# Performance work log

Measured on AMD Instinct MI355X. Metric: run time of the kernel, lower is better.

## Reference

```python
import jax, jax.numpy as jnp
import numpy as np

N_O = 50000
N_Q = 50000
E = 1_600_000
POS_DIM = 3
LATENT = 128
HEADS = 4
HEAD_DIM = 32
EDGE_IN = 3 * POS_DIM  # ['rel','q_pos','o_pos']


def setup_inputs() -> dict:
    key = jax.random.key(0)
    ks = jax.random.split(key, 12)
    h_obs = jax.random.normal(ks[0], (N_O, LATENT), dtype=jnp.float32)
    pos_obs = jax.random.uniform(ks[1], (N_O, POS_DIM), dtype=jnp.float32)
    pos_query = jax.random.uniform(ks[2], (N_Q, POS_DIM), dtype=jnp.float32)
    src = jax.random.randint(ks[3], (E,), 0, N_O, dtype=jnp.int32)
    dst = jnp.sort(jax.random.randint(ks[4], (E,), 0, N_Q, dtype=jnp.int32))
    s = 0.05
    W1 = jax.random.normal(ks[5], (EDGE_IN, LATENT), dtype=jnp.float32) * s
    b1 = jnp.zeros((LATENT,), dtype=jnp.float32)
    W2 = jax.random.normal(ks[6], (LATENT, HEADS), dtype=jnp.float32) * s
    b2 = jnp.zeros((HEADS,), dtype=jnp.float32)
    Wv = jax.random.normal(ks[7], (LATENT, HEADS * HEAD_DIM), dtype=jnp.float32) * s
    bv = jnp.zeros((HEADS * HEAD_DIM,), dtype=jnp.float32)
    log_sigma = jnp.float32(-2.0)
    return {"h_obs": h_obs, "pos_obs": pos_obs, "pos_query": pos_query,
            "src": src, "dst": dst,
            "W1": W1, "b1": b1, "W2": W2, "b2": b2,
            "Wv": Wv, "bv": bv, "log_sigma": log_sigma}


def _forward(h_obs, pos_obs, pos_query, src, dst, W1, b1, W2, b2, Wv, bv, log_sigma):
    pos_o = pos_obs[src]                      # [E, P]
    pos_q = pos_query[dst]                    # [E, P]
    rel = pos_q - pos_o
    edge_attr = jnp.concatenate([rel, pos_q, pos_o], axis=-1)   # [E, 3P]
    hid = jax.nn.relu(edge_attr @ W1 + b1)                      # [E, LATENT]
    logits = hid @ W2 + b2                                      # [E, H]
    dist2 = jnp.sum(rel * rel, axis=-1, keepdims=True)          # [E, 1]
    sigma = jnp.exp(log_sigma) + 1e-6
    logits = logits - dist2 / (2.0 * sigma * sigma)             # kernel log-weight
    # segment softmax over edges grouped by dst
    n_q = pos_query.shape[0]
    m = jax.ops.segment_max(logits, dst, num_segments=n_q)      # [N_q, H]
    ex = jnp.exp(logits - m[dst])
    denom = jax.ops.segment_sum(ex, dst, num_segments=n_q)      # [N_q, H]
    attn = ex / (denom[dst] + 1e-16)                            # [E, H]
    v = (h_obs @ Wv + bv).reshape(-1, HEADS, HEAD_DIM)          # [N_o, H, D]
    msg = attn[:, :, None] * v[src]                             # [E, H, D]
    out = jax.ops.segment_sum(msg, dst, num_segments=n_q)       # [N_q, H, D]
    return out.reshape(n_q, HEADS * HEAD_DIM)


def reference(h_obs, pos_obs, pos_query, src, dst, W1, b1, W2, b2, Wv, bv, log_sigma):
    return _forward(h_obs, pos_obs, pos_query, src, dst, W1, b1, W2, b2, Wv, bv, log_sigma)
```

## Files before the change

kernel.cpp:

```cpp
#include <hip/hip_runtime.h>
#include <hip/hip_bf16.h>
#include <cstdint>
#include <cstddef>

#define N_O 50000
#define N_Q 50000
#define NE  1600000

#define EDGE_BLOCKS  (NE / 64)
#define VP_BLOCKS    ((N_O + 31) / 32)
#define RP_BLOCKS    ((N_Q + 128) / 128)
#define WCAP 264

#define WVP_OFF   38608768u
#define WVP_BYTES 65536u

typedef __attribute__((ext_vector_type(8)))  short short8;
typedef __attribute__((ext_vector_type(16))) float f32x16;

__device__ inline unsigned short f2bf(float x) {
    __hip_bfloat16 hb = __float2bfloat16(x);
    return *reinterpret_cast<unsigned short*>(&hb);
}

__device__ inline unsigned pk2(float a, float b) {
    __hip_bfloat162 t = __float22bfloat162_rn(make_float2(a, b));
    return *reinterpret_cast<unsigned*>(&t);
}

__global__ void pack_kernel(const float* __restrict__ W1, const float* __restrict__ b1,
                            const float* __restrict__ W2, const float* __restrict__ b2,
                            const float* __restrict__ log_sigma,
                            const float* __restrict__ Wv,
                            unsigned short* __restrict__ W1cT,
                            unsigned short* __restrict__ W2tb,
                            float* __restrict__ scal,
                            unsigned short* __restrict__ WvPhi,
                            unsigned short* __restrict__ WvPlo,
                            int vp_mfma) {
    int j = threadIdx.x;
    if (blockIdx.x == 0) {
        if (j < 128) {
            #pragma unroll
            for (int a = 0; a < 3; ++a) {
                W1cT[j * 8 + a]     = f2bf(W1[(3 + a) * 128 + j] + W1[a * 128 + j]);
                W1cT[j * 8 + 3 + a] = f2bf(W1[(6 + a) * 128 + j] - W1[a * 128 + j]);
            }
            W1cT[j * 8 + 6] = f2bf(b1[j]);
            W1cT[j * 8 + 7] = 0;
            #pragma unroll
            for (int hd = 0; hd < 4; ++hd)
                W2tb[hd * 128 + j] = f2bf(W2[j * 4 + hd]);
        } else if (j == 128) {
            float sigma = expf(log_sigma[0]) + 1e-6f;
            scal[0] = 1.0f / (2.0f * sigma * sigma);
            scal[1] = b2[0]; scal[2] = b2[1]; scal[3] = b2[2]; scal[4] = b2[3];
        }
    } else if (vp_mfma) {
        int fr = (blockIdx.x - 1) * 256 + j;
        int lane = fr & 63, i = lane & 31, g = lane >> 5;
        int ks = (fr >> 6) & 7, c = fr >> 9;
        #pragma unroll
        for (int e = 0; e < 8; ++e) {
            float w = Wv[(size_t)(16 * ks + 8 * g + e) * 128 + 32 * c + i];
            unsigned short hi = f2bf(w);
            float rem = w - __uint_as_float(((unsigned)hi) << 16);
            WvPhi[fr * 8 + e] = hi;
            WvPlo[fr * 8 + e] = f2bf(rem);
        }
    }
}

__device__ void rowptr_body(int bid, const int* __restrict__ dst, int* __restrict__ rp) {
    int q = bid * 128 + threadIdx.x;
    if (q > N_Q) return;
    int lo = 0, hi = NE;
    while (lo < hi) {
        int mid = (lo + hi) >> 1;
        if (dst[mid] < q) lo = mid + 1; else hi = mid;
    }
    rp[q] = lo;
}

__device__ void vproj_mfma_body(int tile, const float* __restrict__ h,
                                const unsigned short* __restrict__ WvPhi,
                                const unsigned short* __restrict__ WvPlo,
                                const float* __restrict__ bv,
                                unsigned short* __restrict__ v) {
    int lane = threadIdx.x & 63, wave = threadIdx.x >> 6;
    int i = lane & 31, g = lane >> 5;
    int n = tile * 32 + i;
    bool nok = (n < N_O);
    const float* hrow = h + (size_t)n * 128;

    short8 Bhi[8], Blo[8];
    #pragma unroll
    for (int ks = 0; ks < 8; ++ks) {
        float4 u0 = make_float4(0.f, 0.f, 0.f, 0.f), u1 = u0;
        if (nok) {
            u0 = *(const float4*)(hrow + 16 * ks + 8 * g);
            u1 = *(const float4*)(hrow + 16 * ks + 8 * g + 4);
        }
        float x[8] = {u0.x, u0.y, u0.z, u0.w, u1.x, u1.y, u1.z, u1.w};
        union { unsigned u[4]; short8 s; } ph, pl;
        #pragma unroll
        for (int p = 0; p < 4; ++p) {
            ph.u[p] = pk2(x[2 * p], x[2 * p + 1]);
            float e0 = x[2 * p]     - __uint_as_float(ph.u[p] << 16);
            float e1 = x[2 * p + 1] - __uint_as_float(ph.u[p] & 0xffff0000u);
            pl.u[p] = pk2(e0, e1);
        }
        Bhi[ks] = ph.s; Blo[ks] = pl.s;
    }

    #pragma unroll 1
    for (int cc = 0; cc < 2; ++cc) {
        int c = 2 * wave + cc;
        f32x16 acc;
        #pragma unroll
        for (int k = 0; k < 16; ++k) acc[k] = 0.f;
        #pragma unroll
        for (int ks = 0; ks < 8; ++ks) {
            int fr = (c * 8 + ks) * 64 + lane;
            short8 Ahi = *(const short8*)(WvPhi + fr * 8);
            short8 Alo = *(const short8*)(WvPlo + fr * 8);
            acc = __builtin_amdgcn_mfma_f32_32x32x16_bf16(Ahi, Bhi[ks], acc, 0, 0, 0);
            acc = __builtin_amdgcn_mfma_f32_32x32x16_bf16(Ahi, Blo[ks], acc, 0, 0, 0);
            acc = __builtin_amdgcn_mfma_f32_32x32x16_bf16(Alo, Bhi[ks], acc, 0, 0, 0);
        }
        if (nok) {
            #pragma unroll
            for (int q = 0; q < 4; ++q) {
                int vc = 32 * c + 8 * q + 4 * g;
                float4 bq = *(const float4*)(bv + vc);
                uint2 ov;
                ov.x = pk2(acc[4 * q + 0] + bq.x, acc[4 * q + 1] + bq.y);
                ov.y = pk2(acc[4 * q + 2] + bq.z, acc[4 * q + 3] + bq.w);
                *(uint2*)(v + (size_t)n * 128 + vc) = ov;
            }
        }
    }
}

__device__ void vproj_f32_body(int bid, const float* __restrict__ h,
                               const float* __restrict__ Wv,
                               const float* __restrict__ bv,
                               unsigned short* __restrict__ v,
                               float* Ash ) {
    int t = threadIdx.x;
    int n0 = bid * 32;
    #pragma unroll
    for (int rep = 0; rep < 8; ++rep) {
        int idx = rep * 128 + t;
        int row = idx >> 5, c4 = (idx & 31) * 4;
        float4 val = make_float4(0.f, 0.f, 0.f, 0.f);
        if (n0 + row < N_O) val = *(const float4*)(h + (size_t)(n0 + row) * 128 + c4);
        float* d = &Ash[row * 132 + c4];
        d[0] = val.x; d[1] = val.y; d[2] = val.z; d[3] = val.w;
    }
    __syncthreads();

    int cg = t & 15, rg = t >> 4;
    int c0 = cg * 8, r0 = rg * 4;
    float acc[4][8];
    #pragma unroll
    for (int i = 0; i < 4; ++i)
        #pragma unroll
        for (int j = 0; j < 8; ++j) acc[i][j] = 0.f;

    const float4* Wv4 = (const float4*)Wv;
    for (int k = 0; k < 128; ++k) {
        float4 b0 = Wv4[k * 32 + cg * 2];
        float4 b1v = Wv4[k * 32 + cg * 2 + 1];
        float bb[8] = {b0.x, b0.y, b0.z, b0.w, b1v.x, b1v.y, b1v.z, b1v.w};
        #pragma unroll
        for (int i = 0; i < 4; ++i) {
            float a = Ash[(r0 + i) * 132 + k];
            #pragma unroll
            for (int j = 0; j < 8; ++j) acc[i][j] += a * bb[j];
        }
    }

    float bvv[8];
    #pragma unroll
    for (int j = 0; j < 8; ++j) bvv[j] = bv[c0 + j];
    #pragma unroll
    for (int i = 0; i < 4; ++i) {
        int n = n0 + r0 + i;
        if (n < N_O) {
            uint4 o;
            o.x = pk2(acc[i][0] + bvv[0], acc[i][1] + bvv[1]);
            o.y = pk2(acc[i][2] + bvv[2], acc[i][3] + bvv[3]);
            o.z = pk2(acc[i][4] + bvv[4], acc[i][5] + bvv[5]);
            o.w = pk2(acc[i][6] + bvv[6], acc[i][7] + bvv[7]);
            *(uint4*)(v + (size_t)n * 128 + c0) = o;
        }
    }
}

__device__ void edge_body(int bid, const float* __restrict__ pos_obs,
                          const float* __restrict__ pos_query,
                          const int* __restrict__ src, const int* __restrict__ dst,
                          const unsigned short* __restrict__ W1cT,
                          const unsigned short* __restrict__ W2tb,
                          const float* __restrict__ scal,
                          float* __restrict__ logitsT,
                          unsigned char* smem ) {
    int t = threadIdx.x;
    int wave = t >> 6, lane = t & 63;
    int i = lane & 31, h = lane >> 5;
    unsigned char* myrow = smem + wave * 8448 + i * 264;

    short8 zero8;
    #pragma unroll
    for (int k = 0; k < 8; ++k) zero8[k] = 0;

    short8 a1[4];
    #pragma unroll
    for (int b = 0; b < 4; ++b)
        a1[b] = (h == 0) ? *(const short8*)(W1cT + (32 * b + i) * 8) : zero8;

    short8 a2[8];
    #pragma unroll
    for (int m = 0; m < 8; ++m)
        a2[m] = (i < 4) ? *(const short8*)(W2tb + i * 128 + m * 16 + h * 8) : zero8;

    int e = bid * 64 + wave * 32 + i;
    int s = src[e], d = dst[e];
    float pox = pos_obs[s * 3 + 0], poy = pos_obs[s * 3 + 1], poz = pos_obs[s * 3 + 2];
    float pqx = pos_query[d * 3 + 0], pqy = pos_query[d * 3 + 1], pqz = pos_query[d * 3 + 2];
    float rx = pqx - pox, ry = pqy - poy, rz = pqz - poz;
    float dist2 = rx * rx + ry * ry + rz * rz;

    short8 bea = zero8;
    if (h == 0) {
        bea[0] = (short)f2bf(pqx); bea[1] = (short)f2bf(pqy); bea[2] = (short)f2bf(pqz);
        bea[3] = (short)f2bf(pox); bea[4] = (short)f2bf(poy); bea[5] = (short)f2bf(poz);
        bea[6] = (short)0x3F80;
        bea[7] = 0;
    }

    f32x16 c1[4];
    #pragma unroll
    for (int b = 0; b < 4; ++b) {
        #pragma unroll
        for (int k = 0; k < 16; ++k) c1[b][k] = 0.0f;
        c1[b] = __builtin_amdgcn_mfma_f32_32x32x16_bf16(a1[b], bea, c1[b], 0, 0, 0);
    }

    #pragma unroll
    for (int b = 0; b < 4; ++b) {
        #pragma unroll
        for (int s_ = 0; s_ < 4; ++s_) {
            float x0 = fmaxf(c1[b][4 * s_ + 0], 0.f);
            float x1 = fmaxf(c1[b][4 * s_ + 1], 0.f);
            float x2 = fmaxf(c1[b][4 * s_ + 2], 0.f);
            float x3 = fmaxf(c1[b][4 * s_ + 3], 0.f);
            uint2 w;
            w.x = pk2(x0, x1);
            w.y = pk2(x2, x3);
            *(uint2*)(myrow + 64 * b + 16 * s_ + 8 * h) = w;
        }
    }

    f32x16 c2;
    #pragma unroll
    for (int k = 0; k < 16; ++k) c2[k] = 0.0f;
    #pragma unroll
    for (int m = 0; m < 8; ++m) {
        uint2 lo = *(const uint2*)(myrow + 32 * m + 16 * h);
        uint2 hi = *(const uint2*)(myrow + 32 * m + 16 * h + 8);
        union { unsigned int u[4]; short8 s; } bf;
        bf.u[0] = lo.x; bf.u[1] = lo.y; bf.u[2] = hi.x; bf.u[3] = hi.y;
        c2 = __builtin_amdgcn_mfma_f32_32x32x16_bf16(a2[m], bf.s, c2, 0, 0, 0);
    }

    if (h == 0) {
        float pen = dist2 * scal[0];
        logitsT[0 * NE + e] = c2[0] + scal[1] - pen;
        logitsT[1 * NE + e] = c2[1] + scal[2] - pen;
        logitsT[2 * NE + e] = c2[2] + scal[3] - pen;
        logitsT[3 * NE + e] = c2[3] + scal[4] - pen;
    }
}

__global__ __launch_bounds__(128) void fused_kernel(
        const float* __restrict__ pos_obs, const float* __restrict__ pos_query,
        const int* __restrict__ src, const int* __restrict__ dst,
        const unsigned short* __restrict__ W1cT,
        const unsigned short* __restrict__ W2tb,
        const float* __restrict__ scal, float* __restrict__ logitsT,
        const float* __restrict__ h_obs, const float* __restrict__ Wv,
        const float* __restrict__ bv, unsigned short* __restrict__ vbuf,
        int* __restrict__ rp,
        const unsigned short* __restrict__ WvPhi,
        const unsigned short* __restrict__ WvPlo,
        int vp_mfma) {
    __shared__ __align__(16) unsigned char smem[16896];
    int b = blockIdx.x;
    if (b < EDGE_BLOCKS) {
        edge_body(b, pos_obs, pos_query, src, dst, W1cT, W2tb, scal, logitsT, smem);
    } else if (b < EDGE_BLOCKS + VP_BLOCKS) {
        int tile = b - EDGE_BLOCKS;
        if (vp_mfma) vproj_mfma_body(tile, h_obs, WvPhi, WvPlo, bv, vbuf);
        else         vproj_f32_body(tile, h_obs, Wv, bv, vbuf, (float*)smem);
    } else {
        rowptr_body(b - EDGE_BLOCKS - VP_BLOCKS, dst, rp);
    }
}

__global__ __launch_bounds__(256) void attn_kernel(const __hip_bfloat162* __restrict__ vb,
                                                   const float* __restrict__ logitsT,
                                                   const int* __restrict__ src,
                                                   const int* __restrict__ rp,
                                                   float* __restrict__ out) {
    __shared__ __align__(16) float wsh[4 * 4 * WCAP];
    int t = threadIdx.x;
    int lane = t & 63, wave = t >> 6;
    int q = blockIdx.x * 4 + wave;
    int s0 = rp[q], s1 = rp[q + 1];
    int cnt = s1 - s0;
    int h = lane >> 4, i = lane & 15;
    const float* lp = logitsT + (size_t)h * NE;

    float m = -INFINITY;
    for (int e = s0 + i; e < s1; e += 16) m = fmaxf(m, lp[e]);
    #pragma unroll
    for (int off = 8; off; off >>= 1) m = fmaxf(m, __shfl_xor(m, off));

    float acc0 = 0.f, acc1 = 0.f, r;

    if (cnt <= 256) {
        int s0a = s0 & ~3;
        float* wpb = wsh + wave * (4 * WCAP) + h * WCAP;
        float sum = 0.f;
        for (int e = s0 + i; e < s1; e += 16) {
            float w = __expf(lp[e] - m);
            wpb[e - s0a] = w;
            sum += w;
        }
        #pragma unroll
        for (int off = 8; off; off >>= 1) sum += __shfl_xor(sum, off);
        r = 1.0f / (sum + 1e-16f);

        int e = s0;
        int e1 = (s0 + 3) & ~3; if (e1 > s1) e1 = s1;
        for (; e < e1; ++e) {
            float w = wpb[e - s0a];
            float2 f = __bfloat1622float2(vb[(size_t)src[e] * 64 + lane]);
            acc0 += w * f.x; acc1 += w * f.y;
        }
        for (; e + 4 <= s1; e += 4) {
            float4 w4 = *(const float4*)(wpb + (e - s0a));
            int4 s4 = *(const int4*)(src + e);
            float2 f0 = __bfloat1622float2(vb[(size_t)s4.x * 64 + lane]);
            float2 f1 = __bfloat1622float2(vb[(size_t)s4.y * 64 + lane]);
            float2 f2 = __bfloat1622float2(vb[(size_t)s4.z * 64 + lane]);
            float2 f3 = __bfloat1622float2(vb[(size_t)s4.w * 64 + lane]);
            acc0 += w4.x * f0.x + w4.y * f1.x + w4.z * f2.x + w4.w * f3.x;
            acc1 += w4.x * f0.y + w4.y * f1.y + w4.z * f2.y + w4.w * f3.y;
        }
        for (; e < s1; ++e) {
            float w = wpb[e - s0a];
            float2 f = __bfloat1622float2(vb[(size_t)src[e] * 64 + lane]);
            acc0 += w * f.x; acc1 += w * f.y;
        }
    } else {
        float sum = 0.f;
        for (int e = s0 + i; e < s1; e += 16) sum += __expf(lp[e] - m);
        #pragma unroll
        for (int off = 8; off; off >>= 1) sum += __shfl_xor(sum, off);
        r = 1.0f / (sum + 1e-16f);

        int e = s0;
        for (; e < s1 && (e & 3); ++e) {
            float w = __expf(lp[e] - m);
            float2 f = __bfloat1622float2(vb[(size_t)src[e] * 64 + lane]);
            acc0 += w * f.x; acc1 += w * f.y;
        }
        for (; e + 4 <= s1; e += 4) {
            float4 l4 = *(const float4*)(lp + e);
            int4 s4 = *(const int4*)(src + e);
            float w0 = __expf(l4.x - m);
            float w1 = __expf(l4.y - m);
            float w2 = __expf(l4.z - m);
            float w3 = __expf(l4.w - m);
            float2 f0 = __bfloat1622float2(vb[(size_t)s4.x * 64 + lane]);
            float2 f1 = __bfloat1622float2(vb[(size_t)s4.y * 64 + lane]);
            float2 f2 = __bfloat1622float2(vb[(size_t)s4.z * 64 + lane]);
            float2 f3 = __bfloat1622float2(vb[(size_t)s4.w * 64 + lane]);
            acc0 += w0 * f0.x + w1 * f1.x + w2 * f2.x + w3 * f3.x;
            acc1 += w0 * f0.y + w1 * f1.y + w2 * f2.y + w3 * f3.y;
        }
        for (; e < s1; ++e) {
            float w = __expf(lp[e] - m);
            float2 f = __bfloat1622float2(vb[(size_t)src[e] * 64 + lane]);
            acc0 += w * f.x; acc1 += w * f.y;
        }
    }
    *(float2*)(out + (size_t)q * 128 + lane * 2) = make_float2(acc0 * r, acc1 * r);
}

extern "C" void kernel_launch(void* const* d_in, const int* in_sizes, int n_in,
                              void* d_out, int out_size, void* d_ws, size_t ws_size,
                              hipStream_t stream) {
    const float* h_obs     = (const float*)d_in[0];
    const float* pos_obs   = (const float*)d_in[1];
    const float* pos_query = (const float*)d_in[2];
    const int*   src       = (const int*)d_in[3];
    const int*   dst       = (const int*)d_in[4];
    const float* W1        = (const float*)d_in[5];
    const float* b1        = (const float*)d_in[6];
    const float* W2        = (const float*)d_in[7];
    const float* b2        = (const float*)d_in[8];
    const float* Wv        = (const float*)d_in[9];
    const float* bv        = (const float*)d_in[10];
    const float* log_sigma = (const float*)d_in[11];
    float* out = (float*)d_out;

    char* ws = (char*)d_ws;
    int*            rp      = (int*)(ws + 0);
    float*          scal    = (float*)(ws + 200192);
    unsigned short* W1cT    = (unsigned short*)(ws + 200256);
    unsigned short* W2tb    = (unsigned short*)(ws + 202304);
    unsigned short* vbuf    = (unsigned short*)(ws + 208640);
    float*          logitsT = (float*)(ws + 13008768);
    unsigned short* WvPhi   = (unsigned short*)(ws + WVP_OFF);
    unsigned short* WvPlo   = (unsigned short*)(ws + WVP_OFF + 32768);

    int vp_mfma = (ws_size >= (size_t)WVP_OFF + WVP_BYTES) ? 1 : 0;

    hipLaunchKernelGGL(pack_kernel, dim3(9), dim3(256), 0, stream,
                       W1, b1, W2, b2, log_sigma, Wv, W1cT, W2tb, scal,
                       WvPhi, WvPlo, vp_mfma);
    hipLaunchKernelGGL(fused_kernel, dim3(EDGE_BLOCKS + VP_BLOCKS + RP_BLOCKS),
                       dim3(128), 0, stream,
                       pos_obs, pos_query, src, dst, W1cT, W2tb, scal, logitsT,
                       h_obs, Wv, bv, vbuf, rp, WvPhi, WvPlo, vp_mfma);
    hipLaunchKernelGGL(attn_kernel, dim3(N_Q / 4), dim3(256), 0, stream,
                       (const __hip_bfloat162*)vbuf, logitsT, src, rp, out);
}
```

Before: 244.7 us.

## Process 64 edges per wave in edge MLP and unroll gather loops by eight

The edge MLP now has each wave handle 64 edges instead of 32. Every lane gathers positions for its own edge, and lane shuffles feed two MFMA passes, so the per-edge index and position loads use the whole wave and the edge block count halves. The second-layer MFMA chain is split into two independent accumulators to shorten the dependency chain. The aggregation loops gain an eight-wide unrolled stage that keeps more independent gathers in flight. Launch bounds now request higher occupancy, which can increase register pressure.

```diff
diff --git a/kernel.cpp b/kernel.cpp
--- a/kernel.cpp
+++ b/kernel.cpp
@@ -7,7 +7,7 @@
 #define N_Q 50000
 #define NE  1600000
 
-#define EDGE_BLOCKS  (NE / 64)
+#define EDGE_BLOCKS  (NE / 128)
 #define VP_BLOCKS    ((N_O + 31) / 32)
 #define RP_BLOCKS    ((N_Q + 128) / 128)
 #define WCAP 264
@@ -215,76 +215,99 @@
     #pragma unroll
     for (int k = 0; k < 8; ++k) zero8[k] = 0;
 
-    short8 a1[4];
-    #pragma unroll
-    for (int b = 0; b < 4; ++b)
-        a1[b] = (h == 0) ? *(const short8*)(W1cT + (32 * b + i) * 8) : zero8;
-
-    short8 a2[8];
-    #pragma unroll
-    for (int m = 0; m < 8; ++m)
-        a2[m] = (i < 4) ? *(const short8*)(W2tb + i * 128 + m * 16 + h * 8) : zero8;
-
-    int e = bid * 64 + wave * 32 + i;
+    int e = bid * 128 + wave * 64 + lane;
     int s = src[e], d = dst[e];
     float pox = pos_obs[s * 3 + 0], poy = pos_obs[s * 3 + 1], poz = pos_obs[s * 3 + 2];
     float pqx = pos_query[d * 3 + 0], pqy = pos_query[d * 3 + 1], pqz = pos_query[d * 3 + 2];
     float rx = pqx - pox, ry = pqy - poy, rz = pqz - poz;
     float dist2 = rx * rx + ry * ry + rz * rz;
 
-    short8 bea = zero8;
-    if (h == 0) {
-        bea[0] = (short)f2bf(pqx); bea[1] = (short)f2bf(pqy); bea[2] = (short)f2bf(pqz);
-        bea[3] = (short)f2bf(pox); bea[4] = (short)f2bf(poy); bea[5] = (short)f2bf(poz);
-        bea[6] = (short)0x3F80;
-        bea[7] = 0;
-    }
-
-    f32x16 c1[4];
-    #pragma unroll
-    for (int b = 0; b < 4; ++b) {
-        #pragma unroll
-        for (int k = 0; k < 16; ++k) c1[b][k] = 0.0f;
-        c1[b] = __builtin_amdgcn_mfma_f32_32x32x16_bf16(a1[b], bea, c1[b], 0, 0, 0);
-    }
-
-    #pragma unroll
-    for (int b = 0; b < 4; ++b) {
-        #pragma unroll
-        for (int s_ = 0; s_ < 4; ++s_) {
-            float x0 = fmaxf(c1[b][4 * s_ + 0], 0.f);
-            float x1 = fmaxf(c1[b][4 * s_ + 1], 0.f);
-            float x2 = fmaxf(c1[b][4 * s_ + 2], 0.f);
-            float x3 = fmaxf(c1[b][4 * s_ + 3], 0.f);
-            uint2 w;
-            w.x = pk2(x0, x1);
-            w.y = pk2(x2, x3);
-            *(uint2*)(myrow + 64 * b + 16 * s_ + 8 * h) = w;
-        }
-    }
-
-    f32x16 c2;
-    #pragma unroll
-    for (int k = 0; k < 16; ++k) c2[k] = 0.0f;
-    #pragma unroll
-    for (int m = 0; m < 8; ++m) {
-        uint2 lo = *(const uint2*)(myrow + 32 * m + 16 * h);
-        uint2 hi = *(const uint2*)(myrow + 32 * m + 16 * h + 8);
-        union { unsigned int u[4]; short8 s; } bf;
-        bf.u[0] = lo.x; bf.u[1] = lo.y; bf.u[2] = hi.x; bf.u[3] = hi.y;
-        c2 = __builtin_amdgcn_mfma_f32_32x32x16_bf16(a2[m], bf.s, c2, 0, 0, 0);
-    }
-
-    if (h == 0) {
-        float pen = dist2 * scal[0];
-        logitsT[0 * NE + e] = c2[0] + scal[1] - pen;
-        logitsT[1 * NE + e] = c2[1] + scal[2] - pen;
-        logitsT[2 * NE + e] = c2[2] + scal[3] - pen;
-        logitsT[3 * NE + e] = c2[3] + scal[4] - pen;
-    }
-}
-
-__global__ __launch_bounds__(128) void fused_kernel(
+    unsigned pk[4];
+    pk[0] = pk2(pqx, pqy);
+    pk[1] = pk2(pqz, pox);
+    pk[2] = pk2(poy, poz);
+    pk[3] = 0x00003F80u;
+
+    unsigned pb[4];
+    #pragma unroll
+    for (int p = 0; p < 4; ++p) pb[p] = (unsigned)__shfl_xor((int)pk[p], 32);
+
+    union { unsigned u[4]; short8 s8; } beaA, beaB;
+    #pragma unroll
+    for (int p = 0; p < 4; ++p) {
+        beaA.u[p] = h ? 0u : pk[p];
+        beaB.u[p] = h ? 0u : pb[p];
+    }
+
+    short8 a1[4];
+    #pragma unroll
+    for (int b = 0; b < 4; ++b)
+        a1[b] = (h == 0) ? *(const short8*)(W1cT + (32 * b + i) * 8) : zero8;
+
+    short8 a2[8];
+    #pragma unroll
+    for (int m = 0; m < 8; ++m)
+        a2[m] = (i < 4) ? *(const short8*)(W2tb + i * 128 + m * 16 + h * 8) : zero8;
+
+    float headA[4], headB[4];
+
+    #pragma unroll
+    for (int set = 0; set < 2; ++set) {
+        const short8 bea = set ? beaB.s8 : beaA.s8;
+
+        f32x16 c1[4];
+        #pragma unroll
+        for (int b = 0; b < 4; ++b) {
+            #pragma unroll
+            for (int k = 0; k < 16; ++k) c1[b][k] = 0.0f;
+            c1[b] = __builtin_amdgcn_mfma_f32_32x32x16_bf16(a1[b], bea, c1[b], 0, 0, 0);
+        }
+
+        #pragma unroll
+        for (int b = 0; b < 4; ++b) {
+            #pragma unroll
+            for (int s_ = 0; s_ < 4; ++s_) {
+                float x0 = fmaxf(c1[b][4 * s_ + 0], 0.f);
+                float x1 = fmaxf(c1[b][4 * s_ + 1], 0.f);
+                float x2 = fmaxf(c1[b][4 * s_ + 2], 0.f);
+                float x3 = fmaxf(c1[b][4 * s_ + 3], 0.f);
+                uint2 w;
+                w.x = pk2(x0, x1);
+                w.y = pk2(x2, x3);
+                *(uint2*)(myrow + 64 * b + 16 * s_ + 8 * h) = w;
+            }
+        }
+
+        f32x16 cx, cy;
+        #pragma unroll
+        for (int k = 0; k < 16; ++k) { cx[k] = 0.0f; cy[k] = 0.0f; }
+        #pragma unroll
+        for (int m = 0; m < 8; m += 2) {
+            uint2 lo0 = *(const uint2*)(myrow + 32 * m + 16 * h);
+            uint2 hi0 = *(const uint2*)(myrow + 32 * m + 16 * h + 8);
+            uint2 lo1 = *(const uint2*)(myrow + 32 * (m + 1) + 16 * h);
+            uint2 hi1 = *(const uint2*)(myrow + 32 * (m + 1) + 16 * h + 8);
+            union { unsigned int u[4]; short8 s; } b0, b1u;
+            b0.u[0] = lo0.x; b0.u[1] = lo0.y; b0.u[2] = hi0.x; b0.u[3] = hi0.y;
+            b1u.u[0] = lo1.x; b1u.u[1] = lo1.y; b1u.u[2] = hi1.x; b1u.u[3] = hi1.y;
+            cx = __builtin_amdgcn_mfma_f32_32x32x16_bf16(a2[m],     b0.s,  cx, 0, 0, 0);
+            cy = __builtin_amdgcn_mfma_f32_32x32x16_bf16(a2[m + 1], b1u.s, cy, 0, 0, 0);
+        }
+        float* hd = set ? headB : headA;
+        #pragma unroll
+        for (int r = 0; r < 4; ++r) hd[r] = cx[r] + cy[r];
+    }
+
+    float pen = dist2 * scal[0];
+    #pragma unroll
+    for (int r = 0; r < 4; ++r) {
+        float vB = __shfl_xor(headB[r], 32);
+        float val = (h ? vB : headA[r]) + scal[1 + r] - pen;
+        logitsT[(size_t)r * NE + e] = val;
+    }
+}
+
+__global__ __launch_bounds__(128, 4) void fused_kernel(
         const float* __restrict__ pos_obs, const float* __restrict__ pos_query,
         const int* __restrict__ src, const int* __restrict__ dst,
         const unsigned short* __restrict__ W1cT,
@@ -350,6 +373,24 @@
             float2 f = __bfloat1622float2(vb[(size_t)src[e] * 64 + lane]);
             acc0 += w * f.x; acc1 += w * f.y;
         }
+        for (; e + 8 <= s1; e += 8) {
+            float4 wa = *(const float4*)(wpb + (e - s0a));
+            float4 wb = *(const float4*)(wpb + (e - s0a) + 4);
+            int4 sa = *(const int4*)(src + e);
+            int4 sb = *(const int4*)(src + e + 4);
+            float2 f0 = __bfloat1622float2(vb[(size_t)sa.x * 64 + lane]);
+            float2 f1 = __bfloat1622float2(vb[(size_t)sa.y * 64 + lane]);
+            float2 f2 = __bfloat1622float2(vb[(size_t)sa.z * 64 + lane]);
+            float2 f3 = __bfloat1622float2(vb[(size_t)sa.w * 64 + lane]);
+            float2 f4 = __bfloat1622float2(vb[(size_t)sb.x * 64 + lane]);
+            float2 f5 = __bfloat1622float2(vb[(size_t)sb.y * 64 + lane]);
+            float2 f6 = __bfloat1622float2(vb[(size_t)sb.z * 64 + lane]);
+            float2 f7 = __bfloat1622float2(vb[(size_t)sb.w * 64 + lane]);
+            acc0 += wa.x * f0.x + wa.y * f1.x + wa.z * f2.x + wa.w * f3.x
+                  + wb.x * f4.x + wb.y * f5.x + wb.z * f6.x + wb.w * f7.x;
+            acc1 += wa.x * f0.y + wa.y * f1.y + wa.z * f2.y + wa.w * f3.y
+                  + wb.x * f4.y + wb.y * f5.y + wb.z * f6.y + wb.w * f7.y;
+        }
         for (; e + 4 <= s1; e += 4) {
             float4 w4 = *(const float4*)(wpb + (e - s0a));
             int4 s4 = *(const int4*)(src + e);
@@ -377,6 +418,28 @@
             float w = __expf(lp[e] - m);
             float2 f = __bfloat1622float2(vb[(size_t)src[e] * 64 + lane]);
             acc0 += w * f.x; acc1 += w * f.y;
+        }
+        for (; e + 8 <= s1; e += 8) {
+            float4 la = *(const float4*)(lp + e);
+            float4 lb = *(const float4*)(lp + e + 4);
+            int4 sa = *(const int4*)(src + e);
+            int4 sb = *(const int4*)(src + e + 4);
+            float w0 = __expf(la.x - m), w1 = __expf(la.y - m);
+            float w2 = __expf(la.z - m), w3 = __expf(la.w - m);
+            float w4 = __expf(lb.x - m), w5 = __expf(lb.y - m);
+            float w6 = __expf(lb.z - m), w7 = __expf(lb.w - m);
+            float2 f0 = __bfloat1622float2(vb[(size_t)sa.x * 64 + lane]);
+            float2 f1 = __bfloat1622float2(vb[(size_t)sa.y * 64 + lane]);
+            float2 f2 = __bfloat1622float2(vb[(size_t)sa.z * 64 + lane]);
+            float2 f3 = __bfloat1622float2(vb[(size_t)sa.w * 64 + lane]);
+            float2 f4 = __bfloat1622float2(vb[(size_t)sb.x * 64 + lane]);
+            float2 f5 = __bfloat1622float2(vb[(size_t)sb.y * 64 + lane]);
+            float2 f6 = __bfloat1622float2(vb[(size_t)sb.z * 64 + lane]);
+            float2 f7 = __bfloat1622float2(vb[(size_t)sb.w * 64 + lane]);
+            acc0 += w0 * f0.x + w1 * f1.x + w2 * f2.x + w3 * f3.x
+                  + w4 * f4.x + w5 * f5.x + w6 * f6.x + w7 * f7.x;
+            acc1 += w0 * f0.y + w1 * f1.y + w2 * f2.y + w3 * f3.y
+                  + w4 * f4.y + w5 * f5.y + w6 * f6.y + w7 * f7.y;
         }
         for (; e + 4 <= s1; e += 4) {
             float4 l4 = *(const float4*)(lp + e);
```

Measured after the change: 207.8 us. 15.1% less time.
